# Optimization experiments

Measured on AMD Instinct MI355X. Metric: run time of the kernel, lower is better.

## Reference

```python
import jax, jax.numpy as jnp
import numpy as np

D = 256        # d_model
DL = 256       # d_latent
S = 2048       # seq_len
B = 8          # batches
F = 8192       # facts per batch (padded)
MAXPOS = 4096
MAXPRED = 1024
NROLE = 64 + 2 # role_emb rows


def setup_inputs() -> dict:
    key = jax.random.key(0)
    ks = jax.random.split(key, 16)
    def nrm(k, shape, s=0.02):
        return jax.random.normal(k, shape, jnp.float32) * s
    return {
        "pos_emb": nrm(ks[0], (MAXPOS, D)),
        "pred_emb": nrm(ks[1], (MAXPRED, D)),
        "role_emb": nrm(ks[2], (NROLE, D)),
        "w1": nrm(ks[3], (3 * D, 2 * D)), "b1": jnp.zeros((2 * D,), jnp.float32),
        "w2": nrm(ks[4], (2 * D, D)),     "b2": jnp.zeros((D,), jnp.float32),
        "ln_g": jnp.ones((D,), jnp.float32), "ln_b": jnp.zeros((D,), jnp.float32),
        "lw1": nrm(ks[5], (D, DL)), "lb1": jnp.zeros((DL,), jnp.float32),
        "lw2": nrm(ks[6], (DL, DL)), "lb2": jnp.zeros((DL,), jnp.float32),
        "pred_idx": jax.random.randint(ks[7], (B, F), 0, MAXPRED),
        "a0": jax.random.randint(ks[8], (B, F), 0, S),
        "a1": jax.random.randint(ks[9], (B, F), 0, S),
        "role_idx": jax.random.randint(ks[10], (B, F), 0, NROLE),
        "is_role": jax.random.randint(ks[11], (B, F), 0, 2).astype(jnp.int32),
        "add_rev": jax.random.randint(ks[12], (B, F), 0, 2).astype(jnp.int32),
        "mask": jax.random.randint(ks[13], (B, F), 0, 2).astype(jnp.int32),
        "seq_len": S,
    }


def reference(pos_emb, pred_emb, role_emb, w1, b1, w2, b2, ln_g, ln_b,
              lw1, lb1, lw2, lb2,
              pred_idx, a0, a1, role_idx, is_role, add_rev, mask, seq_len):
    nodes = pos_emb[:seq_len]                 # [S, D] shared across batches
    pe = pred_emb[pred_idx]                   # [B, F, D]
    n0 = nodes[a0]                            # [B, F, D]
    n1 = nodes[a1]                            # [B, F, D]
    re = role_emb[role_idx]                   # [B, F, D]

    role_b = is_role.astype(bool)
    valid = mask.astype(bool)

    third = jnp.where(role_b[..., None], re, n1)
    x_fwd = jnp.concatenate([n0, pe, third], axis=-1)   # [B, F, 3D]
    x_rev = jnp.concatenate([n1, pe, n0], axis=-1)      # [B, F, 3D]

    def mlp(x):
        h = jax.nn.gelu(x @ w1 + b1, approximate=False)
        return h @ w2 + b2

    msg_fwd = mlp(x_fwd)                      # [B, F, D]
    msg_rev = mlp(x_rev)                      # [B, F, D]

    w_fwd = valid[..., None].astype(msg_fwd.dtype)
    w_rev = (valid & (~role_b) & add_rev.astype(bool))[..., None].astype(msg_rev.dtype)
    tgt_fwd = jnp.where(role_b, a0, a1)       # role msgs go to tok=a0, binary to a1

    def scat(msg, idx, w):
        return jax.ops.segment_sum(msg * w, idx, num_segments=seq_len)

    agg = jax.vmap(scat)(msg_fwd, tgt_fwd, w_fwd)
    agg = agg + jax.vmap(scat)(msg_rev, a0, w_rev)      # [B, S, D]

    x = nodes[None, :, :] + agg
    mu = jnp.mean(x, axis=-1, keepdims=True)
    var = jnp.mean(jnp.square(x - mu), axis=-1, keepdims=True)
    x = (x - mu) / jnp.sqrt(var + 1e-5) * ln_g + ln_b   # LayerNorm

    pooled = jnp.mean(x, axis=1)              # [B, D]
    h = jax.nn.gelu(pooled @ lw1 + lb1, approximate=False)
    return h @ lw2 + lb2                      # [B, DL]
```

## Files before the change

### kernel.cpp

```cpp
#include <hip/hip_runtime.h>
#include <hip/hip_bf16.h>
#include <cstdint>

#define S_LEN 2048
#define DIM   256
#define NBAT  8
#define NEDGE 65536
#define HID   512
#define INDIM 768

#define OFF_AGG   0u
#define OFF_POOL  16777216u
#define OFF_CNT   16785408u
#define OFF_NODES 16785664u
#define OFF_PRED  17834240u
#define OFF_ROLE  18358528u
#define OFF_W1P   18392576u
#define OFF_W2P   19179008u
#define OFF_FWD   19441152u
#define OFF_REV   19703296u

typedef short bshort8 __attribute__((ext_vector_type(8)));
typedef float floatx4 __attribute__((ext_vector_type(4)));
typedef ushort ushort4v __attribute__((ext_vector_type(4)));

__device__ __forceinline__ float gelu_f(float x) {
  return 0.5f * x * (1.0f + erff(x * 0.70710678118654752f));
}
__device__ __forceinline__ ushort f2bf(float v) {
  __hip_bfloat16 h = __float2bfloat16(v);
  return *reinterpret_cast<ushort*>(&h);
}

#define Z4 1049088
#define T4 200832
#define WN 524288
#define FLAT_BLOCKS 6931
__global__ void prep_build(const float* __restrict__ pos, const float* __restrict__ pred,
                           const float* __restrict__ role,
                           const float* __restrict__ w1, const float* __restrict__ w2,
                           const int* __restrict__ mask, const int* __restrict__ is_role,
                           const int* __restrict__ add_rev,
                           unsigned char* __restrict__ ws) {
  if (blockIdx.x >= FLAT_BLOCKS) {
    __shared__ int wc0[4], wc1[4], base[2];
    int* fwd = (int*)(ws + OFF_FWD);
    int* rev = (int*)(ws + OFF_REV);
    int* cnt = (int*)(ws + OFF_CNT);
    int tid = threadIdx.x;
    int e = (blockIdx.x - FLAT_BLOCKS) * 256 + tid;
    int lane = tid & 63, w = tid >> 6;
    bool c0 = mask[e] != 0;
    bool c1 = c0 && !is_role[e] && add_rev[e];
    unsigned long long b0 = __ballot(c0);
    unsigned long long b1m = __ballot(c1);
    unsigned long long lt = (1ull << lane) - 1ull;
    if (lane == 0) { wc0[w] = __popcll(b0); wc1[w] = __popcll(b1m); }
    __syncthreads();
    if (tid == 0) {
      base[0] = atomicAdd(&cnt[0], wc0[0] + wc0[1] + wc0[2] + wc0[3]);
      base[1] = atomicAdd(&cnt[1], wc1[0] + wc1[1] + wc1[2] + wc1[3]);
    }
    __syncthreads();
    int p0 = base[0], p1 = base[1];
    for (int ww = 0; ww < 4; ++ww)
      if (ww < w) { p0 += wc0[ww]; p1 += wc1[ww]; }
    if (c0) fwd[p0 + __popcll(b0 & lt)] = e;
    if (c1) rev[p1 + __popcll(b1m & lt)] = e;
    return;
  }
  int i = blockIdx.x * 256 + threadIdx.x;
  if (i < Z4) {
    reinterpret_cast<float4*>(ws)[i] = float4{0.f, 0.f, 0.f, 0.f};
    return;
  }
  i -= Z4;
  if (i < T4) {
    const int NN4 = 131072, NP4 = 65536;
    float4 v;
    if (i < NN4) v = reinterpret_cast<const float4*>(pos)[i];
    else if (i < NN4 + NP4) v = reinterpret_cast<const float4*>(pred)[i - NN4];
    else v = reinterpret_cast<const float4*>(role)[i - NN4 - NP4];
    ushort4v h;
    h.x = f2bf(v.x); h.y = f2bf(v.y); h.z = f2bf(v.z); h.w = f2bf(v.w);
    *reinterpret_cast<ushort4v*>((ushort*)(ws + OFF_NODES) + (i << 2)) = h;
    return;
  }
  i -= T4;
  if (i < WN) {
    ushort* W1p = (ushort*)(ws + OFF_W1P);
    ushort* W2p = (ushort*)(ws + OFF_W2P);
    const int N1 = INDIM * HID;
    if (i < N1) {
      int k = i >> 9, n = i & 511;
      W1p[(((k >> 3) << 9) + n) * 8 + (k & 7)] = f2bf(w1[i]);
    } else {
      int j = i - N1;
      int k = j >> 8, n = j & 255;
      W2p[(((k >> 3) << 8) + n) * 8 + (k & 7)] = f2bf(w2[j]);
    }
  }
}

#define HSTR2 264
__global__ __launch_bounds__(512, 4)
void mlp_kernel(const int* __restrict__ cnt, const int* __restrict__ fwd, const int* __restrict__ rev,
                const int* __restrict__ a0, const int* __restrict__ a1,
                const int* __restrict__ pred_idx, const int* __restrict__ role_idx,
                const int* __restrict__ is_role,
                const ushort* __restrict__ T,
                const ushort* __restrict__ W1p, const ushort* __restrict__ W2p,
                const float* __restrict__ b1, const float* __restrict__ b2,
                float* __restrict__ agg) {
  __shared__ ushort Hs[64 * HSTR2];
  __shared__ int ltgt[64];
  __shared__ int lbat[64];
  __shared__ uint loff[64][3];

  const int tid = threadIdx.x;
  const int nf = cnt[0], nr = cnt[1];
  const int total = nf + nr;
  const int row0 = blockIdx.x * 64;
  if (row0 >= total) return;

  if (tid < 64) {
    int grow = row0 + tid;
    int tgt = -1, bb = 0; uint o0 = 0, o1 = 0, o2 = 0;
    if (grow < total) {
      bool rv = grow >= nf;
      int e = rv ? rev[grow - nf] : fwd[grow];
      bb = e >> 13;
      int A0 = a0[e], A1 = a1[e];
      o1 = 524288u + ((uint)pred_idx[e] << 8);
      if (rv)              { o0 = (uint)A1 << 8; o2 = (uint)A0 << 8;                      tgt = A0; }
      else if (is_role[e]) { o0 = (uint)A0 << 8; o2 = 786432u + ((uint)role_idx[e] << 8); tgt = A0; }
      else                 { o0 = (uint)A0 << 8; o2 = (uint)A1 << 8;                      tgt = A1; }
    }
    ltgt[tid] = tgt; lbat[tid] = bb;
    loff[tid][0] = o0; loff[tid][1] = o1; loff[tid][2] = o2;
  }
  __syncthreads();

  const int lane = tid & 63, wave = tid >> 6;
  const int wm = wave >> 2, wn = wave & 3;
  const int l15 = lane & 15, kb = lane >> 4;
  const int kcb = kb * 8;
  const int m0 = wm * 32 + l15;
  const int m1 = m0 + 16;

  const uint o00 = loff[m0][0], o01 = loff[m0][1], o02 = loff[m0][2];
  const uint o10 = loff[m1][0], o11 = loff[m1][1], o12 = loff[m1][2];

  floatx4 acc2[2][4];
#pragma unroll
  for (int fm = 0; fm < 2; ++fm)
#pragma unroll
    for (int fn = 0; fn < 4; ++fn) acc2[fm][fn] = (floatx4){0.f, 0.f, 0.f, 0.f};

#pragma unroll 1
  for (int h = 0; h < 2; ++h) {
    const int nb = h * 256 + wn * 64;

    floatx4 acc1[2][4];
#pragma unroll
    for (int fm = 0; fm < 2; ++fm)
#pragma unroll
      for (int fn = 0; fn < 4; ++fn) acc1[fm][fn] = (floatx4){0.f, 0.f, 0.f, 0.f};

    bshort8 xb0 = *reinterpret_cast<const bshort8*>(T + o00 + kcb);
    bshort8 xb1 = *reinterpret_cast<const bshort8*>(T + o10 + kcb);
#pragma unroll 1
    for (int k0 = 0; k0 < INDIM; k0 += 32) {
      int k1 = k0 + 32;
      uint po0 = (k1 < 256) ? o00 : (k1 < 512) ? o01 : o02;
      uint po1 = (k1 < 256) ? o10 : (k1 < 512) ? o11 : o12;
      int kc1 = (k1 & 255) + kcb;
      bshort8 nx0 = *reinterpret_cast<const bshort8*>(T + po0 + kc1);
      bshort8 nx1 = *reinterpret_cast<const bshort8*>(T + po1 + kc1);

      const ushort* wp = W1p + ((((k0 >> 3) + kb) << 9) + nb + l15) * 8;
#pragma unroll
      for (int fn = 0; fn < 4; ++fn) {
        bshort8 wv = *reinterpret_cast<const bshort8*>(wp + (fn << 7));
        acc1[0][fn] = __builtin_amdgcn_mfma_f32_16x16x32_bf16(wv, xb0, acc1[0][fn], 0, 0, 0);
        acc1[1][fn] = __builtin_amdgcn_mfma_f32_16x16x32_bf16(wv, xb1, acc1[1][fn], 0, 0, 0);
      }
      xb0 = nx0; xb1 = nx1;
    }

#pragma unroll
    for (int fm = 0; fm < 2; ++fm) {
      int m = fm ? m1 : m0;
#pragma unroll
      for (int fn = 0; fn < 4; ++fn) {
        int nl = wn * 64 + fn * 16 + kb * 4;
        float4 bb4 = *reinterpret_cast<const float4*>(b1 + nb + fn * 16 + kb * 4);
        floatx4 a = fm ? acc1[1][fn] : acc1[0][fn];
        ushort4v hv;
        hv.x = f2bf(gelu_f(a[0] + bb4.x));
        hv.y = f2bf(gelu_f(a[1] + bb4.y));
        hv.z = f2bf(gelu_f(a[2] + bb4.z));
        hv.w = f2bf(gelu_f(a[3] + bb4.w));
        *reinterpret_cast<ushort4v*>(Hs + m * HSTR2 + nl) = hv;
      }
    }
    __syncthreads();

#pragma unroll 1
    for (int kl = 0; kl < 256; kl += 32) {
      bshort8 ha0 = *reinterpret_cast<const bshort8*>(Hs + m0 * HSTR2 + kl + kcb);
      bshort8 ha1 = *reinterpret_cast<const bshort8*>(Hs + m1 * HSTR2 + kl + kcb);
      int kg = h * 256 + kl;
      const ushort* wp2 = W2p + ((((kg >> 3) + kb) << 8) + wn * 64 + l15) * 8;
#pragma unroll
      for (int fn = 0; fn < 4; ++fn) {
        bshort8 wv = *reinterpret_cast<const bshort8*>(wp2 + (fn << 7));
        acc2[0][fn] = __builtin_amdgcn_mfma_f32_16x16x32_bf16(ha0, wv, acc2[0][fn], 0, 0, 0);
        acc2[1][fn] = __builtin_amdgcn_mfma_f32_16x16x32_bf16(ha1, wv, acc2[1][fn], 0, 0, 0);
      }
    }
    __syncthreads();
  }

#pragma unroll
  for (int fn = 0; fn < 4; ++fn) {
    int n = wn * 64 + fn * 16 + l15;
    float bias = b2[n];
#pragma unroll
    for (int fm = 0; fm < 2; ++fm) {
#pragma unroll
      for (int rg = 0; rg < 4; ++rg) {
        int m = wm * 32 + fm * 16 + kb * 4 + rg;
        int tgt = ltgt[m];
        if (tgt >= 0) {
          unsafeAtomicAdd(agg + ((((uint)lbat[m] << 11) + (uint)tgt) << 8) + n,
                          acc2[fm][fn][rg] + bias);
        }
      }
    }
  }
}

__global__ void ln_pool_final(const float* __restrict__ pos, const float* __restrict__ agg,
                              const float* __restrict__ g, const float* __restrict__ be,
                              float* __restrict__ pooled_sum, int* __restrict__ cnt,
                              const float* __restrict__ lw1, const float* __restrict__ lb1,
                              const float* __restrict__ lw2, const float* __restrict__ lb2,
                              float* __restrict__ out) {
  __shared__ float r2[16];
  __shared__ int s_old;
  __shared__ float pl[8 * 256];
  __shared__ float hl[8 * 256];
  const int b = blockIdx.x >> 7;
  const int sb = blockIdx.x & 127;
  const int t = threadIdx.x;
  const float gg = g[t], bb = be[t];
  const int wv = t >> 6;
  float psum = 0.f;
#pragma unroll 1
  for (int i = 0; i < 16; ++i) {
    int s = sb * 16 + i;
    float x = pos[s * DIM + t] + agg[((b << 11) + s) * DIM + t];
    float a = x, q = x * x;
#pragma unroll
    for (int o = 32; o > 0; o >>= 1) { a += __shfl_xor(a, o); q += __shfl_xor(q, o); }
    if ((t & 63) == 0) { r2[wv * 2] = a; r2[wv * 2 + 1] = q; }
    __syncthreads();
    a = r2[0] + r2[2] + r2[4] + r2[6];
    q = r2[1] + r2[3] + r2[5] + r2[7];
    __syncthreads();
    float mu = a * (1.f / 256.f);
    float var = q * (1.f / 256.f) - mu * mu;
    float y = (x - mu) * rsqrtf(var + 1e-5f) * gg + bb;
    psum += y;
  }
  unsafeAtomicAdd(&pooled_sum[(b << 8) + t], psum);
  __syncthreads();
  if (t == 0) {
    __threadfence();
    s_old = atomicAdd(&cnt[2], 1);
  }
  __syncthreads();
  if (s_old != 1023) return;

  for (int i = t; i < 2048; i += 256)
    pl[i] = atomicAdd(&pooled_sum[i], 0.0f) * (1.f / 2048.f);
  __syncthreads();
  float acc[8];
#pragma unroll
  for (int r = 0; r < 8; ++r) acc[r] = lb1[t];
  for (int d = 0; d < 256; ++d) {
    float w = lw1[(d << 8) + t];
#pragma unroll
    for (int r = 0; r < 8; ++r) acc[r] = fmaf(pl[(r << 8) + d], w, acc[r]);
  }
#pragma unroll
  for (int r = 0; r < 8; ++r) hl[(r << 8) + t] = gelu_f(acc[r]);
  __syncthreads();
#pragma unroll
  for (int r = 0; r < 8; ++r) acc[r] = lb2[t];
  for (int d = 0; d < 256; ++d) {
    float w = lw2[(d << 8) + t];
#pragma unroll
    for (int r = 0; r < 8; ++r) acc[r] = fmaf(hl[(r << 8) + d], w, acc[r]);
  }
#pragma unroll
  for (int r = 0; r < 8; ++r) out[(r << 8) + t] = acc[r];
}

extern "C" void kernel_launch(void* const* d_in, const int* in_sizes, int n_in,
                              void* d_out, int out_size, void* d_ws, size_t ws_size,
                              hipStream_t stream) {
  const float* pos_emb  = (const float*)d_in[0];
  const float* pred_emb = (const float*)d_in[1];
  const float* role_emb = (const float*)d_in[2];
  const float* w1   = (const float*)d_in[3];
  const float* b1   = (const float*)d_in[4];
  const float* w2   = (const float*)d_in[5];
  const float* b2   = (const float*)d_in[6];
  const float* ln_g = (const float*)d_in[7];
  const float* ln_b = (const float*)d_in[8];
  const float* lw1  = (const float*)d_in[9];
  const float* lb1  = (const float*)d_in[10];
  const float* lw2  = (const float*)d_in[11];
  const float* lb2  = (const float*)d_in[12];
  const int* pred_idx = (const int*)d_in[13];
  const int* a0       = (const int*)d_in[14];
  const int* a1       = (const int*)d_in[15];
  const int* role_idx = (const int*)d_in[16];
  const int* is_role  = (const int*)d_in[17];
  const int* add_rev  = (const int*)d_in[18];
  const int* mask     = (const int*)d_in[19];

  unsigned char* ws = (unsigned char*)d_ws;
  float*  agg    = (float*)(ws + OFF_AGG);
  float*  pooled = (float*)(ws + OFF_POOL);
  int*    cnt    = (int*)(ws + OFF_CNT);
  ushort* T      = (ushort*)(ws + OFF_NODES);
  ushort* W1p    = (ushort*)(ws + OFF_W1P);
  ushort* W2p    = (ushort*)(ws + OFF_W2P);
  int*    fwd    = (int*)(ws + OFF_FWD);
  int*    rev    = (int*)(ws + OFF_REV);

  hipMemsetAsync(ws + OFF_CNT, 0, 64, stream);
  prep_build<<<FLAT_BLOCKS + 256, 256, 0, stream>>>(pos_emb, pred_emb, role_emb, w1, w2,
                                                    mask, is_role, add_rev, ws);
  mlp_kernel<<<2048, 512, 0, stream>>>(cnt, fwd, rev, a0, a1, pred_idx, role_idx, is_role,
                                       T, W1p, W2p, b1, b2, agg);
  ln_pool_final<<<1024, 256, 0, stream>>>(pos_emb, agg, ln_g, ln_b, pooled, cnt,
                                          lw1, lb1, lw2, lb2, (float*)d_out);
}
```

Baseline: 310.6 us.

## Stage X and weight tiles through double-buffered LDS with async global_load_lds

The MLP kernel now fuses both GEMM phases into one flat 64-step loop. Each step prefetches the next step's gathered activation tile and W1/W2 weight tile into a double-buffered LDS region using global_load_lds, so global latency overlaps the MFMA work and weights are shared across waves instead of each wave loading them from global memory. In exchange the kernel uses much more LDS (about 40KB extra per block), which may reduce occupancy under launch_bounds(512,4). It also depends on the barriers around the buffer swaps being correct.

New measurement: 319.8 us. +3.0%, slower.

```diff
diff --git a/kernel.cpp b/kernel.cpp
--- a/kernel.cpp
+++ b/kernel.cpp
@@ -23,6 +23,13 @@
 typedef short bshort8 __attribute__((ext_vector_type(8)));
 typedef float floatx4 __attribute__((ext_vector_type(4)));
 typedef ushort ushort4v __attribute__((ext_vector_type(4)));
+
+typedef __attribute__((address_space(1))) const unsigned char* gas_t;
+typedef __attribute__((address_space(3))) unsigned char* las_t;
+
+__device__ __forceinline__ void gload_lds16(const ushort* g, ushort* l) {
+  __builtin_amdgcn_global_load_lds((gas_t)g, (las_t)l, 16, 0, 0);
+}
 
 __device__ __forceinline__ float gelu_f(float x) {
   return 0.5f * x * (1.0f + erff(x * 0.70710678118654752f));
@@ -102,7 +109,6 @@
   }
 }
 
-#define HSTR2 264
 __global__ __launch_bounds__(512, 4)
 void mlp_kernel(const int* __restrict__ cnt, const int* __restrict__ fwd, const int* __restrict__ rev,
                 const int* __restrict__ a0, const int* __restrict__ a1,
@@ -112,7 +118,9 @@
                 const ushort* __restrict__ W1p, const ushort* __restrict__ W2p,
                 const float* __restrict__ b1, const float* __restrict__ b2,
                 float* __restrict__ agg) {
-  __shared__ ushort Hs[64 * HSTR2];
+  __shared__ __align__(16) ushort XsA[2][2048];
+  __shared__ __align__(16) ushort WsA[2][8192];
+  __shared__ __align__(16) ushort Hs[64 * 264];
   __shared__ int ltgt[64];
   __shared__ int lbat[64];
   __shared__ uint loff[64][3];
@@ -148,73 +156,91 @@
   const int m0 = wm * 32 + l15;
   const int m1 = m0 + 16;
 
-  const uint o00 = loff[m0][0], o01 = loff[m0][1], o02 = loff[m0][2];
-  const uint o10 = loff[m1][0], o11 = loff[m1][1], o12 = loff[m1][2];
-
-  floatx4 acc2[2][4];
+  if (wave < 4)
+    gload_lds16(T + loff[lane][0] + wave * 8, &XsA[0][wave * 512]);
+#pragma unroll
+  for (int p = 0; p < 2; ++p) {
+    int within = (wave & 1) * 1024 + p * 512 + lane * 8;
+    gload_lds16(W1p + (wave >> 1) * 4096 + within, &WsA[0][wave * 1024 + p * 512]);
+  }
+  __syncthreads();
+
+  floatx4 acc1[2][4], acc2[2][4];
 #pragma unroll
   for (int fm = 0; fm < 2; ++fm)
 #pragma unroll
     for (int fn = 0; fn < 4; ++fn) acc2[fm][fn] = (floatx4){0.f, 0.f, 0.f, 0.f};
 
 #pragma unroll 1
-  for (int h = 0; h < 2; ++h) {
-    const int nb = h * 256 + wn * 64;
-
-    floatx4 acc1[2][4];
-#pragma unroll
-    for (int fm = 0; fm < 2; ++fm)
-#pragma unroll
-      for (int fn = 0; fn < 4; ++fn) acc1[fm][fn] = (floatx4){0.f, 0.f, 0.f, 0.f};
-
-    bshort8 xb0 = *reinterpret_cast<const bshort8*>(T + o00 + kcb);
-    bshort8 xb1 = *reinterpret_cast<const bshort8*>(T + o10 + kcb);
-#pragma unroll 1
-    for (int k0 = 0; k0 < INDIM; k0 += 32) {
-      int k1 = k0 + 32;
-      uint po0 = (k1 < 256) ? o00 : (k1 < 512) ? o01 : o02;
-      uint po1 = (k1 < 256) ? o10 : (k1 < 512) ? o11 : o12;
-      int kc1 = (k1 & 255) + kcb;
-      bshort8 nx0 = *reinterpret_cast<const bshort8*>(T + po0 + kc1);
-      bshort8 nx1 = *reinterpret_cast<const bshort8*>(T + po1 + kc1);
-
-      const ushort* wp = W1p + ((((k0 >> 3) + kb) << 9) + nb + l15) * 8;
+  for (int g = 0; g < 64; ++g) {
+    const int b = g & 1;
+    const int gn = g + 1;
+    if (gn < 64) {
+      const int sh = gn >> 5, sn = gn & 31;
+      ushort* xd = &XsA[b ^ 1][0];
+      ushort* wd = &WsA[b ^ 1][0];
+      if (sn < 24) {
+        const int k0 = sn * 32;
+        if (wave < 4)
+          gload_lds16(T + loff[lane][k0 >> 8] + (k0 & 255) + wave * 8, xd + wave * 512);
+#pragma unroll
+        for (int p = 0; p < 2; ++p) {
+          int within = (wave & 1) * 1024 + p * 512 + lane * 8;
+          gload_lds16(W1p + ((k0 >> 3) + (wave >> 1)) * 4096 + sh * 2048 + within,
+                      wd + wave * 1024 + p * 512);
+        }
+      } else {
+        const int kg = sh * 256 + (sn - 24) * 32;
+#pragma unroll
+        for (int p = 0; p < 2; ++p) {
+          int o = wave * 1024 + p * 512 + lane * 8;
+          gload_lds16(W2p + (kg >> 3) * 2048 + o, wd + wave * 1024 + p * 512);
+        }
+      }
+    }
+    const int s = g & 31, h = g >> 5;
+    const ushort* xs = &XsA[b][0];
+    const ushort* wsp = &WsA[b][0];
+    if (s < 24) {
+      if (s == 0) {
+#pragma unroll
+        for (int fm = 0; fm < 2; ++fm)
+#pragma unroll
+          for (int fn = 0; fn < 4; ++fn) acc1[fm][fn] = (floatx4){0.f, 0.f, 0.f, 0.f};
+      }
+      bshort8 xb0 = *reinterpret_cast<const bshort8*>(xs + kb * 512 + m0 * 8);
+      bshort8 xb1 = *reinterpret_cast<const bshort8*>(xs + kb * 512 + m1 * 8);
 #pragma unroll
       for (int fn = 0; fn < 4; ++fn) {
-        bshort8 wv = *reinterpret_cast<const bshort8*>(wp + (fn << 7));
+        bshort8 wv = *reinterpret_cast<const bshort8*>(wsp + kb * 2048 + (wn * 64 + fn * 16 + l15) * 8);
         acc1[0][fn] = __builtin_amdgcn_mfma_f32_16x16x32_bf16(wv, xb0, acc1[0][fn], 0, 0, 0);
         acc1[1][fn] = __builtin_amdgcn_mfma_f32_16x16x32_bf16(wv, xb1, acc1[1][fn], 0, 0, 0);
       }
-      xb0 = nx0; xb1 = nx1;
-    }
-
-#pragma unroll
-    for (int fm = 0; fm < 2; ++fm) {
-      int m = fm ? m1 : m0;
+      if (s == 23) {
+#pragma unroll
+        for (int fm = 0; fm < 2; ++fm) {
+          int m = fm ? m1 : m0;
+#pragma unroll
+          for (int fn = 0; fn < 4; ++fn) {
+            int nl = wn * 64 + fn * 16 + kb * 4;
+            float4 bb4 = *reinterpret_cast<const float4*>(b1 + h * 256 + nl);
+            floatx4 a = acc1[fm][fn];
+            ushort4v hv;
+            hv.x = f2bf(gelu_f(a[0] + bb4.x));
+            hv.y = f2bf(gelu_f(a[1] + bb4.y));
+            hv.z = f2bf(gelu_f(a[2] + bb4.z));
+            hv.w = f2bf(gelu_f(a[3] + bb4.w));
+            *reinterpret_cast<ushort4v*>(Hs + m * 264 + nl) = hv;
+          }
+        }
+      }
+    } else {
+      const int kl = (s - 24) * 32;
+      bshort8 ha0 = *reinterpret_cast<const bshort8*>(Hs + m0 * 264 + kl + kcb);
+      bshort8 ha1 = *reinterpret_cast<const bshort8*>(Hs + m1 * 264 + kl + kcb);
 #pragma unroll
       for (int fn = 0; fn < 4; ++fn) {
-        int nl = wn * 64 + fn * 16 + kb * 4;
-        float4 bb4 = *reinterpret_cast<const float4*>(b1 + nb + fn * 16 + kb * 4);
-        floatx4 a = fm ? acc1[1][fn] : acc1[0][fn];
-        ushort4v hv;
-        hv.x = f2bf(gelu_f(a[0] + bb4.x));
-        hv.y = f2bf(gelu_f(a[1] + bb4.y));
-        hv.z = f2bf(gelu_f(a[2] + bb4.z));
-        hv.w = f2bf(gelu_f(a[3] + bb4.w));
-        *reinterpret_cast<ushort4v*>(Hs + m * HSTR2 + nl) = hv;
-      }
-    }
-    __syncthreads();
-
-#pragma unroll 1
-    for (int kl = 0; kl < 256; kl += 32) {
-      bshort8 ha0 = *reinterpret_cast<const bshort8*>(Hs + m0 * HSTR2 + kl + kcb);
-      bshort8 ha1 = *reinterpret_cast<const bshort8*>(Hs + m1 * HSTR2 + kl + kcb);
-      int kg = h * 256 + kl;
-      const ushort* wp2 = W2p + ((((kg >> 3) + kb) << 8) + wn * 64 + l15) * 8;
-#pragma unroll
-      for (int fn = 0; fn < 4; ++fn) {
-        bshort8 wv = *reinterpret_cast<const bshort8*>(wp2 + (fn << 7));
+        bshort8 wv = *reinterpret_cast<const bshort8*>(wsp + kb * 2048 + (wn * 64 + fn * 16 + l15) * 8);
         acc2[0][fn] = __builtin_amdgcn_mfma_f32_16x16x32_bf16(ha0, wv, acc2[0][fn], 0, 0, 0);
         acc2[1][fn] = __builtin_amdgcn_mfma_f32_16x16x32_bf16(ha1, wv, acc2[1][fn], 0, 0, 0);
       }
```

## Replace per-message float atomics with bucketed message slots gathered in LayerNorm

Applied to the files above, without the earlier changes.

Adds a histogram kernel that counts messages per (batch, token), builds an exclusive prefix sum in the last compaction block, and gives each MLP row a slot through an atomic on a write pointer. The MLP epilogue then writes message vectors with plain stores into a slot buffer instead of doing 256 float atomics per row into agg. The LayerNorm kernel sums each token's messages by looping over its bucket, and agg atomics remain as a fallback only when a slot exceeds the capacity. This trades global atomic contention for an extra kernel, a 64 MB message buffer write and read, and a serial per-token gather loop that varies with bucket size.

Measured after the change: 361.7 us. +16.4%, slower.

```diff
diff --git a/kernel.cpp b/kernel.cpp
--- a/kernel.cpp
+++ b/kernel.cpp
@@ -19,6 +19,11 @@
 #define OFF_W2P   19179008u
 #define OFF_FWD   19441152u
 #define OFF_REV   19703296u
+#define OFF_HIST  19965440u
+#define OFF_BST   20030976u
+#define OFF_WPTR  20096512u
+#define OFF_MSG   20971520u
+#define MSGCAP    65536
 
 typedef short bshort8 __attribute__((ext_vector_type(8)));
 typedef float floatx4 __attribute__((ext_vector_type(4)));
@@ -30,6 +35,20 @@
 __device__ __forceinline__ ushort f2bf(float v) {
   __hip_bfloat16 h = __float2bfloat16(v);
   return *reinterpret_cast<ushort*>(&h);
+}
+
+__global__ void hist_kernel(const int* __restrict__ mask, const int* __restrict__ is_role,
+                            const int* __restrict__ add_rev,
+                            const int* __restrict__ a0, const int* __restrict__ a1,
+                            int* __restrict__ hist) {
+  int e = blockIdx.x * 256 + threadIdx.x;
+  if (e >= NEDGE) return;
+  if (!mask[e]) return;
+  int bb = e >> 13;
+  int ir = is_role[e];
+  int tf = ir ? a0[e] : a1[e];
+  atomicAdd(&hist[(bb << 11) + tf], 1);
+  if (!ir && add_rev[e]) atomicAdd(&hist[(bb << 11) + a0[e]], 1);
 }
 
 #define Z4 1049088
@@ -43,10 +62,12 @@
                            const int* __restrict__ add_rev,
                            unsigned char* __restrict__ ws) {
   if (blockIdx.x >= FLAT_BLOCKS) {
-    __shared__ int wc0[4], wc1[4], base[2];
-    int* fwd = (int*)(ws + OFF_FWD);
-    int* rev = (int*)(ws + OFF_REV);
-    int* cnt = (int*)(ws + OFF_CNT);
+    __shared__ int wc0[4], wc1[4], base[2], wsum[4];
+    __shared__ int s_last;
+    int* fwd  = (int*)(ws + OFF_FWD);
+    int* rev  = (int*)(ws + OFF_REV);
+    int* cnt  = (int*)(ws + OFF_CNT);
+    int* hist = (int*)(ws + OFF_HIST);
     int tid = threadIdx.x;
     int e = (blockIdx.x - FLAT_BLOCKS) * 256 + tid;
     int lane = tid & 63, w = tid >> 6;
@@ -67,6 +88,37 @@
       if (ww < w) { p0 += wc0[ww]; p1 += wc1[ww]; }
     if (c0) fwd[p0 + __popcll(b0 & lt)] = e;
     if (c1) rev[p1 + __popcll(b1m & lt)] = e;
+
+    __threadfence();
+    __syncthreads();
+    if (tid == 0) s_last = atomicAdd(&cnt[3], 1);
+    __syncthreads();
+    if (s_last != 255) return;
+
+    int* bst  = (int*)(ws + OFF_BST);
+    int* wptr = (int*)(ws + OFF_WPTR);
+    int c[64];
+    int sum = 0;
+#pragma unroll
+    for (int j = 0; j < 64; ++j) {
+      c[j] = atomicAdd(&hist[tid * 64 + j], 0);
+      sum += c[j];
+    }
+    int inc = sum;
+    for (int o = 1; o < 64; o <<= 1) {
+      int v = __shfl_up(inc, o);
+      if (lane >= o) inc += v;
+    }
+    if (lane == 63) wsum[w] = inc;
+    __syncthreads();
+    int woff = 0;
+    for (int ww = 0; ww < w; ++ww) woff += wsum[ww];
+    int run = woff + inc - sum;
+#pragma unroll
+    for (int j = 0; j < 64; ++j) {
+      int idx = tid * 64 + j;
+      bst[idx] = run; wptr[idx] = run; run += c[j];
+    }
     return;
   }
   int i = blockIdx.x * 256 + threadIdx.x;
@@ -111,10 +163,11 @@
                 const ushort* __restrict__ T,
                 const ushort* __restrict__ W1p, const ushort* __restrict__ W2p,
                 const float* __restrict__ b1, const float* __restrict__ b2,
-                float* __restrict__ agg) {
+                float* __restrict__ agg, float* __restrict__ msg, int* __restrict__ wptr) {
   __shared__ ushort Hs[64 * HSTR2];
   __shared__ int ltgt[64];
   __shared__ int lbat[64];
+  __shared__ int lslot[64];
   __shared__ uint loff[64][3];
 
   const int tid = threadIdx.x;
@@ -125,7 +178,7 @@
 
   if (tid < 64) {
     int grow = row0 + tid;
-    int tgt = -1, bb = 0; uint o0 = 0, o1 = 0, o2 = 0;
+    int tgt = -1, bb = 0, slot = -1; uint o0 = 0, o1 = 0, o2 = 0;
     if (grow < total) {
       bool rv = grow >= nf;
       int e = rv ? rev[grow - nf] : fwd[grow];
@@ -135,8 +188,9 @@
       if (rv)              { o0 = (uint)A1 << 8; o2 = (uint)A0 << 8;                      tgt = A0; }
       else if (is_role[e]) { o0 = (uint)A0 << 8; o2 = 786432u + ((uint)role_idx[e] << 8); tgt = A0; }
       else                 { o0 = (uint)A0 << 8; o2 = (uint)A1 << 8;                      tgt = A1; }
-    }
-    ltgt[tid] = tgt; lbat[tid] = bb;
+      slot = atomicAdd(&wptr[(bb << 11) + tgt], 1);
+    }
+    ltgt[tid] = tgt; lbat[tid] = bb; lslot[tid] = slot;
     loff[tid][0] = o0; loff[tid][1] = o1; loff[tid][2] = o2;
   }
   __syncthreads();
@@ -194,7 +248,7 @@
 #pragma unroll
       for (int fn = 0; fn < 4; ++fn) {
         int nl = wn * 64 + fn * 16 + kb * 4;
-        float4 bb4 = *reinterpret_cast<const float4*>(b1 + nb + fn * 16 + kb * 4);
+        float4 bb4 = *reinterpret_cast<const float4*>(b1 + h * 256 + nl);
         floatx4 a = fm ? acc1[1][fn] : acc1[0][fn];
         ushort4v hv;
         hv.x = f2bf(gelu_f(a[0] + bb4.x));
@@ -231,10 +285,11 @@
 #pragma unroll
       for (int rg = 0; rg < 4; ++rg) {
         int m = wm * 32 + fm * 16 + kb * 4 + rg;
-        int tgt = ltgt[m];
-        if (tgt >= 0) {
-          unsafeAtomicAdd(agg + ((((uint)lbat[m] << 11) + (uint)tgt) << 8) + n,
-                          acc2[fm][fn][rg] + bias);
+        int sl = lslot[m];
+        if (sl >= 0) {
+          float v = acc2[fm][fn][rg] + bias;
+          if (sl < MSGCAP) msg[(size_t)sl * 256 + n] = v;
+          else unsafeAtomicAdd(agg + ((((uint)lbat[m] << 11) + (uint)ltgt[m]) << 8) + n, v);
         }
       }
     }
@@ -242,6 +297,8 @@
 }
 
 __global__ void ln_pool_final(const float* __restrict__ pos, const float* __restrict__ agg,
+                              const float* __restrict__ msg,
+                              const int* __restrict__ bst, const int* __restrict__ hist,
                               const float* __restrict__ g, const float* __restrict__ be,
                               float* __restrict__ pooled_sum, int* __restrict__ cnt,
                               const float* __restrict__ lw1, const float* __restrict__ lb1,
@@ -260,7 +317,14 @@
 #pragma unroll 1
   for (int i = 0; i < 16; ++i) {
     int s = sb * 16 + i;
-    float x = pos[s * DIM + t] + agg[((b << 11) + s) * DIM + t];
+    int u = (b << 11) + s;
+    float x = pos[s * DIM + t] + agg[((size_t)u << 8) + t];
+    int st = bst[u], cn = hist[u];
+#pragma unroll 1
+    for (int p = 0; p < cn; ++p) {
+      int sl = st + p;
+      if (sl < MSGCAP) x += msg[(size_t)sl * 256 + t];
+    }
     float a = x, q = x * x;
 #pragma unroll
     for (int o = 32; o > 0; o >>= 1) { a += __shfl_xor(a, o); q += __shfl_xor(q, o); }
@@ -341,12 +405,18 @@
   ushort* W2p    = (ushort*)(ws + OFF_W2P);
   int*    fwd    = (int*)(ws + OFF_FWD);
   int*    rev    = (int*)(ws + OFF_REV);
-
-  hipMemsetAsync(ws + OFF_CNT, 0, 64, stream);
+  int*    hist   = (int*)(ws + OFF_HIST);
+  int*    bst    = (int*)(ws + OFF_BST);
+  int*    wptr   = (int*)(ws + OFF_WPTR);
+  float*  msg    = (float*)(ws + OFF_MSG);
+
+  hipMemsetAsync(ws + OFF_CNT, 0, 256, stream);
+  hipMemsetAsync(ws + OFF_HIST, 0, 65536, stream);
+  hist_kernel<<<256, 256, 0, stream>>>(mask, is_role, add_rev, a0, a1, hist);
   prep_build<<<FLAT_BLOCKS + 256, 256, 0, stream>>>(pos_emb, pred_emb, role_emb, w1, w2,
                                                     mask, is_role, add_rev, ws);
   mlp_kernel<<<2048, 512, 0, stream>>>(cnt, fwd, rev, a0, a1, pred_idx, role_idx, is_role,
-                                       T, W1p, W2p, b1, b2, agg);
-  ln_pool_final<<<1024, 256, 0, stream>>>(pos_emb, agg, ln_g, ln_b, pooled, cnt,
-                                          lw1, lb1, lw2, lb2, (float*)d_out);
-}
+                                       T, W1p, W2p, b1, b2, agg, msg, wptr);
+  ln_pool_final<<<1024, 256, 0, stream>>>(pos_emb, agg, msg, bst, hist, ln_g, ln_b,
+                                          pooled, cnt, lw1, lb1, lw2, lb2, (float*)d_out);
+}
```
